# Optimization experiments

Hardware: AMD Instinct MI355X
Metric: run time of the kernel (lower is better)

The kernel has to match this reference:

```python
import jax, jax.numpy as jnp
import numpy as np
from jax import lax

SB, MB = 2, 2          # mb fixed to 2 (original samples randint(1,4))
IMH = IMW = 128
RH = RW = 64           # render resolution
NS = 64                # coarse samples per ray
C, D = 16, 64
HID = 128
BOUND = 3.5            # scene bound for coord normalization
DELTA_LAST = 1e3


def make_rays(k, shape):
    k1, k2 = jax.random.split(k)
    o = 0.1 * jax.random.normal(k1, shape + (3,), jnp.float32)
    d = jax.random.normal(k2, shape + (3,), jnp.float32)
    d = d / jnp.linalg.norm(d, axis=-1, keepdims=True)
    near = jnp.full(shape + (1,), 1.0, jnp.float32)
    far = jnp.full(shape + (1,), 3.0, jnp.float32)
    return jnp.concatenate([o, d, near, far], -1)


def setup_inputs():
    key = jax.random.key(0)
    ks = jax.random.split(key, 10)
    images = jax.random.normal(ks[0], (SB, 3, 3, IMH, IMW), jnp.float32)
    cond_rays = make_rays(ks[1], (SB, 3, RH, RW))
    target_rays = make_rays(ks[2], (SB, 1, RH, RW))
    W_enc = 0.05 * jax.random.normal(ks[3], (C * D, 3, 3, 3), jnp.float32)
    b_enc = jnp.zeros((C * D,), jnp.float32)
    W1 = jax.random.normal(ks[4], (C, HID), jnp.float32) / jnp.sqrt(float(C))
    b1 = jnp.zeros((HID,), jnp.float32)
    W2 = jax.random.normal(ks[5], (HID, HID), jnp.float32) / jnp.sqrt(float(HID))
    b2 = jnp.zeros((HID,), jnp.float32)
    W3 = jax.random.normal(ks[6], (HID, 4), jnp.float32) / jnp.sqrt(float(HID))
    b3 = jnp.zeros((4,), jnp.float32)
    return dict(images=images, cond_rays=cond_rays, target_rays=target_rays,
                W_enc=W_enc, b_enc=b_enc, W1=W1, b1=b1, W2=W2, b2=b2,
                W3=W3, b3=b3, norm_src=0)


def sample_coarse_points(rays):
    # rays: (B, RH, RW, 8)
    o, d = rays[..., 0:3], rays[..., 3:6]
    near, far = rays[..., 6], rays[..., 7]
    t = (jnp.arange(NS, dtype=jnp.float32) + 0.5) / NS
    z = near[..., None] * (1.0 - t) + far[..., None] * t      # (B,RH,RW,NS)
    pts = o[..., None, :] + d[..., None, :] * z[..., None]    # (B,RH,RW,NS,3)
    pts = jnp.moveaxis(pts, 3, 1)                             # (B,NS,RH,RW,3)
    z = jnp.moveaxis(z, 3, 1)                                 # (B,NS,RH,RW)
    deltas = jnp.concatenate([jnp.diff(z, axis=1),
                              jnp.full_like(z[:, :1], DELTA_LAST)], axis=1)
    return pts, deltas, z


def sample_from_3dgrid(vol, pts, cond_pts, norm_src):
    # vol: (B,C,Dv,Hv,Wv); pts: (B,NS,RH,RW,3) world coords -> trilinear sample
    B, Cc, Dv, Hv, Wv = vol.shape
    if norm_src:
        scale = jnp.max(jnp.abs(cond_pts.reshape(B, -1)), axis=1) + 1e-6
        coords = pts / scale[:, None, None, None, None]
    else:
        coords = pts / BOUND
    coords = jnp.clip(coords, -1.0, 1.0).reshape(B, -1, 3)    # (B,N,3) xyz
    ux = (coords[..., 0] + 1.0) * 0.5 * (Wv - 1)
    uy = (coords[..., 1] + 1.0) * 0.5 * (Hv - 1)
    uz = (coords[..., 2] + 1.0) * 0.5 * (Dv - 1)
    x0 = jnp.clip(jnp.floor(ux), 0, Wv - 2).astype(jnp.int32)
    y0 = jnp.clip(jnp.floor(uy), 0, Hv - 2).astype(jnp.int32)
    z0 = jnp.clip(jnp.floor(uz), 0, Dv - 2).astype(jnp.int32)
    fx = ux - x0; fy = uy - y0; fz = uz - z0
    vol_flat = vol.reshape(B, Cc, Dv * Hv * Wv).transpose(0, 2, 1)  # (B,DHW,C)

    def gather(zz, yy, xx):
        idx = (zz * Hv + yy) * Wv + xx                         # (B,N)
        return jnp.take_along_axis(vol_flat, idx[..., None], axis=1)

    out = jnp.zeros(vol_flat.shape[:1] + (coords.shape[1], Cc), vol.dtype)
    for dz in (0, 1):
        wz = fz if dz else (1.0 - fz)
        for dy in (0, 1):
            wy = fy if dy else (1.0 - fy)
            for dx in (0, 1):
                wx = fx if dx else (1.0 - fx)
                w = (wz * wy * wx)[..., None]
                out = out + w * gather(z0 + dz, y0 + dy, x0 + dx)
    return out.reshape(B, NS, RH, RW, Cc)


def composite(feat, deltas, z):
    # feat: (sb,NS,RH,RW,4)
    rgb = jax.nn.sigmoid(feat[..., :3])
    sigma = jax.nn.relu(feat[..., 3])
    alpha = 1.0 - jnp.exp(-sigma * deltas)
    trans = jnp.cumprod(1.0 - alpha + 1e-10, axis=1)
    trans = jnp.concatenate([jnp.ones_like(trans[:, :1]), trans[:, :-1]], axis=1)
    weights = alpha * trans
    rgb_final = jnp.sum(weights[..., None] * rgb, axis=1)     # (sb,RH,RW,3)
    depth_final = jnp.sum(weights * z, axis=1)                # (sb,RH,RW)
    return rgb_final, depth_final


def reference(images, cond_rays, target_rays, W_enc, b_enc, W1, b1, W2, b2, W3, b3, norm_src):
    sb = images.shape[0]; mb = MB
    batch_images = images[:, :mb].reshape(sb * mb, 3, IMH, IMW)
    cond_r = cond_rays[:, :mb].reshape(sb * mb, RH, RW, 8)
    batch_rays = jnp.repeat(target_rays, mb, axis=1).reshape(sb * mb, RH, RW, 8)

    # FeatureVolumeEncoder: conv2d 3 -> C*D, stride 2 (128->64), relu, reshape to 3D volume
    feat2d = lax.conv_general_dilated(batch_images, W_enc, (2, 2), 'SAME',
                                      dimension_numbers=('NCHW', 'OIHW', 'NCHW'))
    feat2d = jax.nn.relu(feat2d + b_enc[None, :, None, None])
    volumes = feat2d.reshape(sb * mb, C, D, 64, 64)

    points, deltas, z_samp = sample_coarse_points(batch_rays)
    cond_points = sample_coarse_points(cond_r)[0] if norm_src else None
    sampled = sample_from_3dgrid(volumes, points, cond_points, norm_src)
    sampled = sampled.reshape(sb, mb, NS, RH, RW, C).mean(axis=1)  # (sb,NS,RH,RW,C)

    # MLP_Nerf: pointwise 16 -> 128 -> 128 -> 4
    x = sampled.reshape(sb, -1, C)
    h = jax.nn.relu(jnp.einsum('bnc,ch->bnh', x, W1) + b1)
    h = jax.nn.relu(jnp.einsum('bnh,hk->bnk', h, W2) + b2)
    feat = (jnp.einsum('bnh,ho->bno', h, W3) + b3).reshape(sb, NS, RH, RW, 4)

    rgb_final, depth_final = composite(feat, deltas[:sb], z_samp[:sb])
    return rgb_final, depth_final
```

## Files before the change

kernel.cpp:

```cpp
#include <hip/hip_runtime.h>
#include <math.h>

typedef __attribute__((ext_vector_type(8))) short short8;
typedef __attribute__((ext_vector_type(4))) short short4v;
typedef __attribute__((ext_vector_type(4))) float f32x4;
typedef __attribute__((ext_vector_type(4))) unsigned int u32x4;

#define OFF_W1 0
#define OFF_W2 16384
#define OFF_W3 81920
#define OFF_B1 83968
#define OFF_B2 84480
#define OFF_B3 84992
#define WPACK_BYTES 86016

__device__ __forceinline__ unsigned short f2bf(float x) {
    union { float f; unsigned u; } v; v.f = x;
    unsigned r = v.u + 0x7FFF + ((v.u >> 16) & 1);
    return (unsigned short)(r >> 16);
}
__device__ __forceinline__ float bf2f(unsigned short h) {
    union { unsigned u; float f; } v; v.u = ((unsigned)h) << 16;
    return v.f;
}
__device__ __forceinline__ float asf(unsigned u) {
    union { unsigned u; float f; } v; v.u = u; return v.f;
}
__device__ __forceinline__ unsigned cvtpk(float a, float b) {
    unsigned d;
    asm("v_cvt_pk_bf16_f32 %0, %1, %2" : "=v"(d) : "v"(a), "v"(b));
    return d;
}
__device__ __forceinline__ unsigned permb(unsigned s0, unsigned s1, unsigned sel) {
    unsigned d;
    asm("v_perm_b32 %0, %1, %2, %3" : "=v"(d) : "v"(s0), "v"(s1), "s"(sel));
    return d;
}

__global__ __launch_bounds__(256) void pack_weights_kernel(
    const float* __restrict__ W1, const float* __restrict__ b1,
    const float* __restrict__ W2, const float* __restrict__ b2,
    const float* __restrict__ W3, const float* __restrict__ b3,
    char* __restrict__ wp)
{
    int s = blockIdx.x * 256 + threadIdx.x;
    if (s >= WPACK_BYTES / 2) return;
    int b = s * 2;
    if (b < OFF_W2) {
        int rr = b >> 7;
        int off = (b & 127) ^ ((rr & 7) << 4);
        int k = (off & 63) >> 1;
        float x = (k < 16) ? W1[k * 128 + rr] : 0.0f;
        unsigned short hi = f2bf(x);
        *(unsigned short*)(wp + b) = (off < 64) ? hi : f2bf(x - bf2f(hi));
    } else if (b < OFF_W3) {
        int i = b - OFF_W2;
        int rr = i >> 9;
        int off = (i & 511) ^ ((rr & 7) << 4);
        int k = (off & 255) >> 1;
        float x = W2[k * 128 + rr];
        unsigned short hi = f2bf(x);
        *(unsigned short*)(wp + b) = (off < 256) ? hi : f2bf(x - bf2f(hi));
    } else if (b < OFF_B1) {
        int i = b - OFF_W3;
        int rr = i >> 9;
        int off = (i & 511) ^ ((rr & 7) << 4);
        int k = (off & 255) >> 1;
        float x = W3[k * 4 + rr];
        unsigned short hi = f2bf(x);
        *(unsigned short*)(wp + b) = (off < 256) ? hi : f2bf(x - bf2f(hi));
    } else if (b < OFF_B3 + 16) {
        if ((b & 3) == 0) {
            float v;
            if (b < OFF_B2)      v = b1[(b - OFF_B1) >> 2];
            else if (b < OFF_B3) v = b2[(b - OFF_B2) >> 2];
            else                 v = b3[(b - OFF_B3) >> 2];
            *(float*)(wp + b) = v;
        }
    } else {
        *(unsigned short*)(wp + b) = 0;
    }
}

__global__ __launch_bounds__(256) void conv_enc_avg_kernel(
    const float* __restrict__ images,
    const float* __restrict__ W_enc,
    const float* __restrict__ b_enc,
    float* __restrict__ vols)
{
    __shared__ float wl[16 * 27];
    __shared__ float bl[16];
    int t = threadIdx.x;
    int gid = blockIdx.x * 256 + t;
    int ow = gid & 63;
    int oh = (gid >> 6) & 63;
    int dz = (gid >> 12) & 63;
    int sb = gid >> 18;

    for (int i = t; i < 16 * 27; i += 256) {
        int c = i / 27, r = i - c * 27;
        wl[i] = W_enc[(c * 64 + dz) * 27 + r];
    }
    if (t < 16) bl[t] = b_enc[t * 64 + dz];
    __syncthreads();

    const float* img0 = images + (size_t)((sb * 3 + 0) * 3) * (128 * 128);
    const float* img1 = images + (size_t)((sb * 3 + 1) * 3) * (128 * 128);

    float acc0[16], acc1[16];
#pragma unroll
    for (int c = 0; c < 16; ++c) { acc0[c] = 0.0f; acc1[c] = 0.0f; }

#pragma unroll
    for (int ci = 0; ci < 3; ++ci) {
#pragma unroll
        for (int kh = 0; kh < 3; ++kh) {
            int ih = oh * 2 + kh;
            if (ih >= 128) continue;
#pragma unroll
            for (int kw = 0; kw < 3; ++kw) {
                int iw = ow * 2 + kw;
                if (iw >= 128) continue;
                float p0 = img0[(ci * 128 + ih) * 128 + iw];
                float p1 = img1[(ci * 128 + ih) * 128 + iw];
                const float* w = &wl[ci * 9 + kh * 3 + kw];
#pragma unroll
                for (int c = 0; c < 16; ++c) {
                    float wv = w[c * 27];
                    acc0[c] = fmaf(p0, wv, acc0[c]);
                    acc1[c] = fmaf(p1, wv, acc1[c]);
                }
            }
        }
    }

    float* outp = vols + ((((size_t)sb * 64 + dz) * 64 + oh) * 64 + ow) * 16;
    float r[16];
#pragma unroll
    for (int c = 0; c < 16; ++c) {
        float v0 = fmaxf(acc0[c] + bl[c], 0.0f);
        float v1 = fmaxf(acc1[c] + bl[c], 0.0f);
        r[c] = (v0 + v1) * 0.5f;
    }
#pragma unroll
    for (int q = 0; q < 4; ++q) {
        float4 v = make_float4(r[q * 4], r[q * 4 + 1], r[q * 4 + 2], r[q * 4 + 3]);
        *(float4*)(outp + q * 4) = v;
    }
}

__device__ __forceinline__ void gather_pt(
    const float* __restrict__ vols, const float* __restrict__ rays,
    int tile, int prow, int cg, float4 cv[8], float wt[8])
{
    int sb = tile >> 12;
    int n0 = (tile & 4095) << 6;
    int n = n0 + prow;
    int i_s = n >> 12, pix = n & 4095;
    const float* ray = rays + ((size_t)sb * 4096 + pix) * 8;
    float ox = ray[0], oy = ray[1], oz = ray[2];
    float rdx = ray[3], rdy = ray[4], rdz = ray[5];
    float nr = ray[6], fr = ray[7];
    float tt = ((float)i_s + 0.5f) * (1.0f / 64.0f);
    float zv = nr * (1.0f - tt) + fr * tt;
    float px = fmaf(rdx, zv, ox);
    float py = fmaf(rdy, zv, oy);
    float pz = fmaf(rdz, zv, oz);
    float cx = fminf(fmaxf(px * (1.0f / 3.5f), -1.0f), 1.0f);
    float cy = fminf(fmaxf(py * (1.0f / 3.5f), -1.0f), 1.0f);
    float cz = fminf(fmaxf(pz * (1.0f / 3.5f), -1.0f), 1.0f);
    float ux = (cx + 1.0f) * 31.5f;
    float uy = (cy + 1.0f) * 31.5f;
    float uz = (cz + 1.0f) * 31.5f;
    int x0 = (int)fminf(floorf(ux), 62.0f);
    int y0 = (int)fminf(floorf(uy), 62.0f);
    int z0 = (int)fminf(floorf(uz), 62.0f);
    float fx = ux - (float)x0;
    float fy = uy - (float)y0;
    float fz = uz - (float)z0;
    float wxa[2] = {1.0f - fx, fx};
    float wya[2] = {1.0f - fy, fy};
    float wza[2] = {1.0f - fz, fz};
    const float* vb = vols + (size_t)sb * (64 * 64 * 64 * 16);
#pragma unroll
    for (int d8 = 0; d8 < 2; ++d8) {
#pragma unroll
        for (int y8 = 0; y8 < 2; ++y8) {
#pragma unroll
            for (int x8 = 0; x8 < 2; ++x8) {
                int i = d8 * 4 + y8 * 2 + x8;
                wt[i] = wza[d8] * wya[y8] * wxa[x8];
                cv[i] = *(const float4*)(vb +
                    ((((size_t)(z0 + d8) * 64) + (y0 + y8)) * 64 + (x0 + x8)) * 16 + cg * 4);
            }
        }
    }
}

__global__ __launch_bounds__(256) void sample_mlp_mfma_kernel(
    const float* __restrict__ vols,
    const float* __restrict__ rays,
    const char* __restrict__ wpack_g,
    float* __restrict__ feat)
{
    __shared__ __align__(16) char sm[126976];
    char* wp = sm;
    char* xs = sm + 86016;
    char* hb = sm + 94208;

    int t = threadIdx.x;

#pragma unroll
    for (int it = 0; it < 21; ++it) {
        int off = it * 4096 + t * 16;
        *(f32x4*)(wp + off) = *(const f32x4*)(wpack_g + off);
    }

    const int w    = t >> 6;
    const int l    = t & 63;
    const int r    = l & 15;
    const int g    = l >> 4;
    const int rb   = w * 16;
    const int prow = rb + r;
    const int swzr = (r & 7) << 4;

    const float* b1s = (const float*)(wp + OFF_B1);
    const float* b2s = (const float*)(wp + OFF_B2);
    const float* b3s = (const float*)(wp + OFF_B3);
    char*       xroww = xs + prow * 128;
    const char* xrow  = xroww;
    const char* hrow  = hb + prow * 512;
    const char* w3row = wp + OFF_W3 + (r & 3) * 512;
    const int   swz3  = (r & 3) << 4;

    {
        short4v zv4; zv4[0] = 0; zv4[1] = 0; zv4[2] = 0; zv4[3] = 0;
        *(short4v*)(xroww + ((32 + g * 8) ^ swzr)) = zv4;
        *(short4v*)(xroww + ((96 + g * 8) ^ swzr)) = zv4;
    }

    __syncthreads();

    float4 cv[8]; float wt[8];
    gather_pt(vols, rays, blockIdx.x, prow, g, cv, wt);

    for (int tile = blockIdx.x; tile < 8192; tile += gridDim.x) {
        const int sb = tile >> 12;
        const int n0 = (tile & 4095) << 6;
        const int nxt = tile + gridDim.x;

        {
            float a0 = 0.f, a1 = 0.f, a2 = 0.f, a3 = 0.f;
#pragma unroll
            for (int i = 0; i < 8; ++i) {
                a0 = fmaf(wt[i], cv[i].x, a0);
                a1 = fmaf(wt[i], cv[i].y, a1);
                a2 = fmaf(wt[i], cv[i].z, a2);
                a3 = fmaf(wt[i], cv[i].w, a3);
            }
            unsigned h01 = cvtpk(a0, a1);
            unsigned h23 = cvtpk(a2, a3);
            float l0 = a0 - asf(h01 << 16);
            float l1 = a1 - asf(h01 & 0xFFFF0000u);
            float l2 = a2 - asf(h23 << 16);
            float l3 = a3 - asf(h23 & 0xFFFF0000u);
            uint2 hv; hv.x = h01; hv.y = h23;
            uint2 lv; lv.x = cvtpk(l0, l1); lv.y = cvtpk(l2, l3);
            *(uint2*)(xroww + ((g * 8) ^ swzr))       = hv;
            *(uint2*)(xroww + ((64 + g * 8) ^ swzr))  = lv;
        }

        short8 xh = *(const short8*)(xrow + ((g * 16) ^ swzr));
        short8 xl = *(const short8*)(xrow + ((64 + g * 16) ^ swzr));
        f32x4 acc1[8];
#pragma unroll
        for (int f = 0; f < 8; ++f) {
            float bv = b1s[16 * f + r];
            f32x4 acc = {bv, bv, bv, bv};
            const char* wrow = wp + OFF_W1 + (16 * f + r) * 128;
            short8 bh = *(const short8*)(wrow + ((g * 16) ^ swzr));
            short8 bl = *(const short8*)(wrow + ((64 + g * 16) ^ swzr));
            acc = __builtin_amdgcn_mfma_f32_16x16x32_bf16(xh, bl, acc, 0, 0, 0);
            acc = __builtin_amdgcn_mfma_f32_16x16x32_bf16(xl, bh, acc, 0, 0, 0);
            acc = __builtin_amdgcn_mfma_f32_16x16x32_bf16(xh, bh, acc, 0, 0, 0);
            acc1[f] = acc;
        }
#pragma unroll
        for (int f = 0; f < 8; ++f) {
#pragma unroll
            for (int q = 0; q < 4; ++q) {
                float v = fmaxf(acc1[f][q], 0.0f);
                unsigned th = cvtpk(v, v);
                float lo = v - asf(th << 16);
                unsigned pk = cvtpk(v, lo);
                int row = rb + 4 * g + q;
                int swzh = (row & 7) << 4;
                *(unsigned*)(hb + row * 512 + ((4 * (16 * f + r)) ^ swzh)) = pk;
            }
        }

        float4 cv2[8]; float wt2[8];
        if (nxt < 8192)
            gather_pt(vols, rays, nxt, prow, g, cv2, wt2);

        f32x4 acc2[8];
#pragma unroll
        for (int f = 0; f < 8; ++f) {
            float bv = b2s[16 * f + r];
            acc2[f] = (f32x4){bv, bv, bv, bv};
        }
#pragma unroll
        for (int s = 0; s < 4; ++s) {
            u32x4 v0 = *(const u32x4*)(hrow + ((s * 128 + g * 32) ^ swzr));
            u32x4 v1 = *(const u32x4*)(hrow + ((s * 128 + g * 32 + 16) ^ swzr));
            union { unsigned w4[4]; short8 s8; } uh, ul;
            uh.w4[0] = permb(v0[1], v0[0], 0x05040100u);
            ul.w4[0] = permb(v0[1], v0[0], 0x07060302u);
            uh.w4[1] = permb(v0[3], v0[2], 0x05040100u);
            ul.w4[1] = permb(v0[3], v0[2], 0x07060302u);
            uh.w4[2] = permb(v1[1], v1[0], 0x05040100u);
            ul.w4[2] = permb(v1[1], v1[0], 0x07060302u);
            uh.w4[3] = permb(v1[3], v1[2], 0x05040100u);
            ul.w4[3] = permb(v1[3], v1[2], 0x07060302u);
            short8 ah = uh.s8, al = ul.s8;
#pragma unroll
            for (int f = 0; f < 8; ++f) {
                const char* wrow = wp + OFF_W2 + (16 * f + r) * 512;
                short8 bh = *(const short8*)(wrow + ((s * 64 + g * 16) ^ swzr));
                short8 bl = *(const short8*)(wrow + ((256 + s * 64 + g * 16) ^ swzr));
                acc2[f] = __builtin_amdgcn_mfma_f32_16x16x32_bf16(ah, bl, acc2[f], 0, 0, 0);
                acc2[f] = __builtin_amdgcn_mfma_f32_16x16x32_bf16(al, bh, acc2[f], 0, 0, 0);
                acc2[f] = __builtin_amdgcn_mfma_f32_16x16x32_bf16(ah, bh, acc2[f], 0, 0, 0);
            }
        }
#pragma unroll
        for (int f = 0; f < 8; ++f) {
#pragma unroll
            for (int q = 0; q < 4; ++q) {
                float v = fmaxf(acc2[f][q], 0.0f);
                unsigned th = cvtpk(v, v);
                float lo = v - asf(th << 16);
                unsigned pk = cvtpk(v, lo);
                int row = rb + 4 * g + q;
                int swzh = (row & 7) << 4;
                *(unsigned*)(hb + row * 512 + ((4 * (16 * f + r)) ^ swzh)) = pk;
            }
        }

        float bv3 = b3s[r & 3];
        f32x4 acc3 = (f32x4){bv3, bv3, bv3, bv3};
#pragma unroll
        for (int s = 0; s < 4; ++s) {
            u32x4 v0 = *(const u32x4*)(hrow + ((s * 128 + g * 32) ^ swzr));
            u32x4 v1 = *(const u32x4*)(hrow + ((s * 128 + g * 32 + 16) ^ swzr));
            union { unsigned w4[4]; short8 s8; } uh, ul;
            uh.w4[0] = permb(v0[1], v0[0], 0x05040100u);
            ul.w4[0] = permb(v0[1], v0[0], 0x07060302u);
            uh.w4[1] = permb(v0[3], v0[2], 0x05040100u);
            ul.w4[1] = permb(v0[3], v0[2], 0x07060302u);
            uh.w4[2] = permb(v1[1], v1[0], 0x05040100u);
            ul.w4[2] = permb(v1[1], v1[0], 0x07060302u);
            uh.w4[3] = permb(v1[3], v1[2], 0x05040100u);
            ul.w4[3] = permb(v1[3], v1[2], 0x07060302u);
            short8 ah = uh.s8, al = ul.s8;
            short8 bh = *(const short8*)(w3row + ((s * 64 + g * 16) ^ swz3));
            short8 bl = *(const short8*)(w3row + ((256 + s * 64 + g * 16) ^ swz3));
            acc3 = __builtin_amdgcn_mfma_f32_16x16x32_bf16(ah, bl, acc3, 0, 0, 0);
            acc3 = __builtin_amdgcn_mfma_f32_16x16x32_bf16(al, bh, acc3, 0, 0, 0);
            acc3 = __builtin_amdgcn_mfma_f32_16x16x32_bf16(ah, bh, acc3, 0, 0, 0);
        }
        if (r < 4) {
            size_t base = ((size_t)sb << 18) + (size_t)(n0 + rb + 4 * g);
#pragma unroll
            for (int q = 0; q < 4; ++q)
                feat[(base + q) * 4 + r] = acc3[q];
        }

        if (nxt < 8192) {
#pragma unroll
            for (int i = 0; i < 8; ++i) { cv[i] = cv2[i]; wt[i] = wt2[i]; }
        }
    }
}

__global__ __launch_bounds__(256) void composite_kernel(
    const float* __restrict__ feat,
    const float* __restrict__ rays,
    float* __restrict__ out)
{
    int gid = blockIdx.x * 256 + threadIdx.x;
    if (gid >= 8192) return;
    int sb = gid >> 12;
    int pix = gid & 4095;
    const float* ray = rays + (size_t)pix * 8;
    float nr = ray[6], fr = ray[7];
    float dstep = (fr - nr) * (1.0f / 64.0f);

    float T = 1.0f;
    float r = 0.f, g = 0.f, b = 0.f, d = 0.f;
    const float* fp = feat + ((size_t)sb * 262144 + pix) * 4;
    for (int i = 0; i < 64; ++i) {
        float4 f = *(const float4*)(fp + (size_t)i * 4096 * 4);
        float rr = 1.0f / (1.0f + expf(-f.x));
        float gg = 1.0f / (1.0f + expf(-f.y));
        float bb = 1.0f / (1.0f + expf(-f.z));
        float sigma = fmaxf(f.w, 0.0f);
        float tt = ((float)i + 0.5f) * (1.0f / 64.0f);
        float zv = nr * (1.0f - tt) + fr * tt;
        float delta = (i == 63) ? 1000.0f : dstep;
        float alpha = 1.0f - expf(-sigma * delta);
        float wgt = alpha * T;
        r += wgt * rr; g += wgt * gg; b += wgt * bb; d += wgt * zv;
        T *= (1.0f - alpha + 1e-10f);
    }
    out[(size_t)gid * 3 + 0] = r;
    out[(size_t)gid * 3 + 1] = g;
    out[(size_t)gid * 3 + 2] = b;
    out[24576 + gid] = d;
}

extern "C" void kernel_launch(void* const* d_in, const int* in_sizes, int n_in,
                              void* d_out, int out_size, void* d_ws, size_t ws_size,
                              hipStream_t stream) {
    const float* images      = (const float*)d_in[0];
    const float* target_rays = (const float*)d_in[2];
    const float* W_enc       = (const float*)d_in[3];
    const float* b_enc       = (const float*)d_in[4];
    const float* W1          = (const float*)d_in[5];
    const float* b1          = (const float*)d_in[6];
    const float* W2          = (const float*)d_in[7];
    const float* b2          = (const float*)d_in[8];
    const float* W3          = (const float*)d_in[9];
    const float* b3          = (const float*)d_in[10];

    float* ws   = (float*)d_ws;
    float* vols = ws;
    float* feat = ws + (size_t)2 * 64 * 64 * 64 * 16;
    char*  wpack = (char*)(feat + (size_t)2 * 262144 * 4);
    float* out  = (float*)d_out;

    pack_weights_kernel<<<168, 256, 0, stream>>>(W1, b1, W2, b2, W3, b3, wpack);
    conv_enc_avg_kernel<<<2048, 256, 0, stream>>>(images, W_enc, b_enc, vols);
    sample_mlp_mfma_kernel<<<256, 256, 0, stream>>>(vols, target_rays, wpack, feat);
    composite_kernel<<<32, 256, 0, stream>>>(feat, target_rays, out);
}
```

Before: 190.4 us.

## Parallelize compositing across samples with wave-level prefix product scan

The compositing kernel now gives each ray a full 64-lane wave, one lane per depth sample, instead of one thread walking 64 samples serially. Transmittance comes from a shuffle-based inclusive prefix product, and the weighted colour and depth are summed with a shuffle-down tree reduction. This replaces a 32-block launch with a long dependent loop by 2048 blocks that expose far more parallelism. The cost is more shuffle instructions and uncoalesced per-lane loads strided by 4096 pixels, plus small floating-point reordering differences.

New measurement: 164.3 us. -13.7%, faster.

```diff
diff --git a/kernel.cpp b/kernel.cpp
--- a/kernel.cpp
+++ b/kernel.cpp
@@ -383,40 +383,59 @@
     }
 }
 
-__global__ __launch_bounds__(256) void composite_kernel(
+__global__ __launch_bounds__(256) void composite_wave_kernel(
     const float* __restrict__ feat,
     const float* __restrict__ rays,
     float* __restrict__ out)
 {
-    int gid = blockIdx.x * 256 + threadIdx.x;
-    if (gid >= 8192) return;
+    int t = threadIdx.x;
+    int lane = t & 63;
+    int gid = blockIdx.x * 4 + (t >> 6);
     int sb = gid >> 12;
     int pix = gid & 4095;
     const float* ray = rays + (size_t)pix * 8;
     float nr = ray[6], fr = ray[7];
     float dstep = (fr - nr) * (1.0f / 64.0f);
 
-    float T = 1.0f;
-    float r = 0.f, g = 0.f, b = 0.f, d = 0.f;
-    const float* fp = feat + ((size_t)sb * 262144 + pix) * 4;
-    for (int i = 0; i < 64; ++i) {
-        float4 f = *(const float4*)(fp + (size_t)i * 4096 * 4);
-        float rr = 1.0f / (1.0f + expf(-f.x));
-        float gg = 1.0f / (1.0f + expf(-f.y));
-        float bb = 1.0f / (1.0f + expf(-f.z));
-        float sigma = fmaxf(f.w, 0.0f);
-        float tt = ((float)i + 0.5f) * (1.0f / 64.0f);
-        float zv = nr * (1.0f - tt) + fr * tt;
-        float delta = (i == 63) ? 1000.0f : dstep;
-        float alpha = 1.0f - expf(-sigma * delta);
-        float wgt = alpha * T;
-        r += wgt * rr; g += wgt * gg; b += wgt * bb; d += wgt * zv;
-        T *= (1.0f - alpha + 1e-10f);
-    }
-    out[(size_t)gid * 3 + 0] = r;
-    out[(size_t)gid * 3 + 1] = g;
-    out[(size_t)gid * 3 + 2] = b;
-    out[24576 + gid] = d;
+    int i = lane;
+    float4 f = *(const float4*)(feat +
+        ((size_t)sb * 262144 + (size_t)i * 4096 + pix) * 4);
+
+    float sigma = fmaxf(f.w, 0.0f);
+    float delta = (i == 63) ? 1000.0f : dstep;
+    float alpha = 1.0f - expf(-sigma * delta);
+    float om = 1.0f - alpha + 1e-10f;
+
+    float prod = om;
+#pragma unroll
+    for (int off = 1; off < 64; off <<= 1) {
+        float v = __shfl_up(prod, off, 64);
+        if (lane >= off) prod *= v;
+    }
+    float T = __shfl_up(prod, 1, 64);
+    if (lane == 0) T = 1.0f;
+    float wgt = alpha * T;
+
+    float tt = ((float)i + 0.5f) * (1.0f / 64.0f);
+    float zv = nr * (1.0f - tt) + fr * tt;
+    float rr = wgt * (1.0f / (1.0f + expf(-f.x)));
+    float gg = wgt * (1.0f / (1.0f + expf(-f.y)));
+    float bb = wgt * (1.0f / (1.0f + expf(-f.z)));
+    float dd = wgt * zv;
+
+#pragma unroll
+    for (int off = 32; off > 0; off >>= 1) {
+        rr += __shfl_down(rr, off, 64);
+        gg += __shfl_down(gg, off, 64);
+        bb += __shfl_down(bb, off, 64);
+        dd += __shfl_down(dd, off, 64);
+    }
+    if (lane == 0) {
+        out[(size_t)gid * 3 + 0] = rr;
+        out[(size_t)gid * 3 + 1] = gg;
+        out[(size_t)gid * 3 + 2] = bb;
+        out[24576 + gid] = dd;
+    }
 }
 
 extern "C" void kernel_launch(void* const* d_in, const int* in_sizes, int n_in,
@@ -442,5 +461,5 @@
     pack_weights_kernel<<<168, 256, 0, stream>>>(W1, b1, W2, b2, W3, b3, wpack);
     conv_enc_avg_kernel<<<2048, 256, 0, stream>>>(images, W_enc, b_enc, vols);
     sample_mlp_mfma_kernel<<<256, 256, 0, stream>>>(vols, target_rays, wpack, feat);
-    composite_kernel<<<32, 256, 0, stream>>>(feat, target_rays, out);
-}
+    composite_wave_kernel<<<2048, 256, 0, stream>>>(feat, target_rays, out);
+}
```
